# Kernel optimization log

Measured on AMD Instinct MI355X. Metric: run time of the kernel, lower is better.

The kernel has to match this reference:

```python
import jax, jax.numpy as jnp
import numpy as np

B, LQ, LK, D, H = 16, 1024, 1024, 512, 8
DK = D // H  # 64
EPS = 1e-5


def _ln(x, g, b):
    m = jnp.mean(x, axis=-1, keepdims=True)
    v = jnp.mean((x - m) ** 2, axis=-1, keepdims=True)
    return (x - m) * jax.lax.rsqrt(v + EPS) * g + b


def _rotate_every_two(x):
    # x: (..., d) with d even; pairs (x1,x2) -> (-x2, x1) interleaved
    x1 = x[..., 0::2]
    x2 = x[..., 1::2]
    return jnp.stack((-x2, x1), axis=-1).reshape(x.shape)


def setup_inputs() -> dict:
    key = jax.random.key(0)
    ks = jax.random.split(key, 16)
    s = 1.0 / np.sqrt(D)
    inp = {
        "satellite": jax.random.normal(ks[0], (B, LK, D), jnp.float32),
        "satellite_pos_embedding": jax.random.normal(ks[1], (2, B, LK, D), jnp.float32),
        "timeseries": jax.random.normal(ks[2], (B, LQ, D), jnp.float32),
        "timeseries_pos_embedding": jax.random.normal(ks[3], (2, B, LQ, D), jnp.float32),
        "ln_sat_g": jnp.ones((D,), jnp.float32),
        "ln_sat_b": jnp.zeros((D,), jnp.float32),
        "ln_ts_g": jnp.ones((D,), jnp.float32),
        "ln_ts_b": jnp.zeros((D,), jnp.float32),
        "Wv": jax.random.normal(ks[4], (D, DK), jnp.float32) * s,
        "bv": jnp.zeros((DK,), jnp.float32),
        "Wq": jax.random.normal(ks[5], (H, D, DK), jnp.float32) * s,
        "bq": jnp.zeros((H, DK), jnp.float32),
        "Wk": jax.random.normal(ks[6], (H, D, DK), jnp.float32) * s,
        "bk": jnp.zeros((H, DK), jnp.float32),
        "Wsat": jax.random.normal(ks[7], (H, D, DK), jnp.float32) * s,
        "bsat": jnp.zeros((H, DK), jnp.float32),
        "Wts": jax.random.normal(ks[8], (H, D, DK), jnp.float32) * s,
        "bts": jnp.zeros((H, DK), jnp.float32),
        "Wh": jax.random.normal(ks[9], (DK, D), jnp.float32) * (1.0 / np.sqrt(DK)),
    }
    return inp


def reference(satellite, satellite_pos_embedding, timeseries, timeseries_pos_embedding,
              ln_sat_g, ln_sat_b, ln_ts_g, ln_ts_b,
              Wv, bv, Wq, bq, Wk, bk, Wsat, bsat, Wts, bts, Wh):
    sat = _ln(satellite, ln_sat_g, ln_sat_b)      # (B,LK,D)
    ts = _ln(timeseries, ln_ts_g, ln_ts_b)        # (B,LQ,D)

    v = ts @ jnp.zeros_like(Wv) if False else sat @ Wv + bv  # (B,LK,DK), shared across heads

    # batched per-head projections
    q = jnp.einsum('bld,hdk->bhlk', ts, Wq) + bq[:, None, :]    # (B,H,LQ,DK)
    k = jnp.einsum('bld,hdk->bhlk', sat, Wk) + bk[:, None, :]   # (B,H,LK,DK)

    sin_sat = jnp.einsum('bld,hdk->bhlk', satellite_pos_embedding[0], Wsat) + bsat[:, None, :]
    cos_sat = jnp.einsum('bld,hdk->bhlk', satellite_pos_embedding[1], Wsat) + bsat[:, None, :]
    sin_ts = jnp.einsum('bld,hdk->bhlk', timeseries_pos_embedding[0], Wts) + bts[:, None, :]
    cos_ts = jnp.einsum('bld,hdk->bhlk', timeseries_pos_embedding[1], Wts) + bts[:, None, :]

    # rotary (dim_rotary == DK, so no pass-through part)
    q = q * cos_ts + _rotate_every_two(q) * sin_ts
    k = k * cos_sat + _rotate_every_two(k) * sin_sat

    scale = jnp.sqrt(jnp.asarray(DK, q.dtype))
    scores = jnp.einsum('bhqd,bhkd->bhqk', q, k) / scale        # (B,H,LQ,LK)
    attn = jax.nn.softmax(scores, axis=-1)
    head = jnp.einsum('bhqk,bkd->bhqd', attn, v)                # (B,H,LQ,DK)

    out = jnp.mean(head, axis=1) @ Wh                           # (B,LQ,D)
    attn_out = jnp.transpose(attn, (0, 2, 1, 3))                # (B,LQ,H,LK) matches torch.stack(dim=2)
    return (out, attn_out)
```

## Files before the change

kernel.cpp:

```cpp
#include <hip/hip_runtime.h>

#define OUT_OFF 8388608ull

typedef __attribute__((ext_vector_type(4))) float f32x4;
typedef __attribute__((ext_vector_type(8))) __bf16 bf16x8;
typedef __attribute__((ext_vector_type(8))) unsigned short us8;

__device__ __forceinline__ unsigned short f2b(float f) {
  return __builtin_bit_cast(unsigned short, (__bf16)f);
}
__device__ __forceinline__ float b2f(unsigned short u) {
  return (float)__builtin_bit_cast(__bf16, u);
}
__device__ __forceinline__ bf16x8 ldfrag(const unsigned short* p) {
  return __builtin_bit_cast(bf16x8, *(const us8*)p);
}
__device__ __forceinline__ f32x4 mfma16(bf16x8 a, bf16x8 b, f32x4 c) {
  return __builtin_amdgcn_mfma_f32_16x16x32_bf16(a, b, c, 0, 0, 0);
}
__device__ __forceinline__ void stage8_f32(unsigned short* dst, const float* src) {
  const f32x4 x = *(const f32x4*)src;
  const f32x4 y = *(const f32x4*)(src + 4);
  us8 v;
  v[0]=f2b(x[0]); v[1]=f2b(x[1]); v[2]=f2b(x[2]); v[3]=f2b(x[3]);
  v[4]=f2b(y[0]); v[5]=f2b(y[1]); v[6]=f2b(y[2]); v[7]=f2b(y[3]);
  *(us8*)dst = v;
}
__device__ __forceinline__ void stage8_split(unsigned short* dh, unsigned short* dl, const float* src) {
  const f32x4 x = *(const f32x4*)src;
  const f32x4 y = *(const f32x4*)(src + 4);
  us8 h, l;
  #pragma unroll
  for (int i = 0; i < 4; ++i) {
    unsigned short hv = f2b(x[i]); h[i] = hv; l[i] = f2b(x[i] - b2f(hv));
  }
  #pragma unroll
  for (int i = 0; i < 4; ++i) {
    unsigned short hv = f2b(y[i]); h[4+i] = hv; l[4+i] = f2b(y[i] - b2f(hv));
  }
  *(us8*)dh = h; *(us8*)dl = l;
}
__device__ __forceinline__ void stage8_bf(unsigned short* dst, const unsigned short* src) {
  *(us8*)dst = *(const us8*)src;
}

__global__ __launch_bounds__(256) void repack_kernel(
    const float* __restrict__ Wq, const float* __restrict__ Wk,
    const float* __restrict__ Wsat, const float* __restrict__ Wts,
    const float* __restrict__ Wv, const float* __restrict__ Wh,
    unsigned short* __restrict__ Wq_h, unsigned short* __restrict__ Wq_l,
    unsigned short* __restrict__ Wk_h, unsigned short* __restrict__ Wk_l,
    unsigned short* __restrict__ Wsat_h, unsigned short* __restrict__ Wsat_l,
    unsigned short* __restrict__ Wts_h, unsigned short* __restrict__ Wts_l,
    float* __restrict__ Wv_t, float* __restrict__ Wh_t)
{
  int i = blockIdx.x * 256 + threadIdx.x;
  if (i < 1048576) {
    int seg = i >> 18, j = i & 262143;
    int n = j >> 9, d = j & 511;
    const float* W = (seg == 0) ? Wq : (seg == 1) ? Wk : (seg == 2) ? Wsat : Wts;
    unsigned short* Oh = (seg == 0) ? Wq_h : (seg == 1) ? Wk_h : (seg == 2) ? Wsat_h : Wts_h;
    unsigned short* Ol = (seg == 0) ? Wq_l : (seg == 1) ? Wk_l : (seg == 2) ? Wsat_l : Wts_l;
    float w = W[((n >> 6) * 512 + d) * 64 + (n & 63)];
    unsigned short h = f2b(w);
    Oh[j] = h; Ol[j] = f2b(w - b2f(h));
  } else if (i < 1081344) {
    int j = i - 1048576; int dk = j >> 9, d = j & 511;
    Wv_t[j] = Wv[d * 64 + dk];
  } else if (i < 1114112) {
    int j = i - 1081344; int d = j >> 6, dk = j & 63;
    Wh_t[j] = Wh[dk * 512 + d];
  }
}

__global__ __launch_bounds__(256) void ln_kernel(
    const float* __restrict__ sat, const float* __restrict__ ts,
    const float* __restrict__ gs, const float* __restrict__ bs,
    const float* __restrict__ gt, const float* __restrict__ bt,
    unsigned short* __restrict__ sat_h, unsigned short* __restrict__ sat_l,
    unsigned short* __restrict__ ts_h, unsigned short* __restrict__ ts_l)
{
  int row = blockIdx.x;
  const float* x; unsigned short *yh, *yl; const float* g; const float* bb;
  if (row < 16384) {
    x = sat + (size_t)row * 512; yh = sat_h + (size_t)row * 512; yl = sat_l + (size_t)row * 512;
    g = gs; bb = bs;
  } else {
    int r = row - 16384;
    x = ts + (size_t)r * 512; yh = ts_h + (size_t)r * 512; yl = ts_l + (size_t)r * 512;
    g = gt; bb = bt;
  }
  int t = threadIdx.x;
  float x0 = x[t], x1 = x[t + 256];
  float s = x0 + x1, s2 = x0 * x0 + x1 * x1;
  #pragma unroll
  for (int o = 1; o < 64; o <<= 1) { s += __shfl_xor(s, o); s2 += __shfl_xor(s2, o); }
  __shared__ float red[8];
  int w = t >> 6;
  if ((t & 63) == 0) { red[w] = s; red[4 + w] = s2; }
  __syncthreads();
  float S  = red[0] + red[1] + red[2] + red[3];
  float S2 = red[4] + red[5] + red[6] + red[7];
  float mean = S * (1.f / 512.f);
  float inv = rsqrtf(S2 * (1.f / 512.f) - mean * mean + 1e-5f);
  float y0 = (x0 - mean) * inv * g[t]       + bb[t];
  float y1 = (x1 - mean) * inv * g[t + 256] + bb[t + 256];
  unsigned short h0 = f2b(y0), h1 = f2b(y1);
  yh[t] = h0;       yl[t] = f2b(y0 - b2f(h0));
  yh[t + 256] = h1; yl[t + 256] = f2b(y1 - b2f(h1));
}

__global__ __launch_bounds__(256) void proj_rope_kernel(
    const unsigned short* __restrict__ Axm_h, const unsigned short* __restrict__ Axm_l,
    const float* __restrict__ Axs, const float* __restrict__ Axc,
    const unsigned short* __restrict__ Bm_h, const unsigned short* __restrict__ Bm_l,
    const unsigned short* __restrict__ Br_h, const unsigned short* __restrict__ Br_l,
    const float* __restrict__ bm_, const float* __restrict__ br_,
    unsigned short* __restrict__ out_h, unsigned short* __restrict__ out_l)
{
  __shared__ __attribute__((aligned(16))) unsigned short
      sAmH[64*40], sAmL[64*40], sAsH[64*40], sAsL[64*40], sAcH[64*40], sAcL[64*40],
      sBmH[64*40], sBmL[64*40], sBrH[64*40], sBrL[64*40];
  const int tid = threadIdx.x;
  const int lane = tid & 63, wid = tid >> 6;
  const int wy = wid >> 1, wx = wid & 1;
  const int m0 = blockIdx.x * 64, n0 = blockIdx.y * 64;
  const int srow = tid >> 2, sc8 = (tid & 3) * 8;
  const int sidx = srow * 40 + sc8;

  f32x4 accM[2][2] = {}, accS[2][2] = {}, accC[2][2] = {};

  for (int k0 = 0; k0 < 512; k0 += 32) {
    const size_t ao = (size_t)(m0 + srow) * 512 + k0 + sc8;
    stage8_bf(&sAmH[sidx], Axm_h + ao);
    stage8_bf(&sAmL[sidx], Axm_l + ao);
    stage8_split(&sAsH[sidx], &sAsL[sidx], Axs + ao);
    stage8_split(&sAcH[sidx], &sAcL[sidx], Axc + ao);
    const size_t bo = (size_t)(n0 + srow) * 512 + k0 + sc8;
    stage8_bf(&sBmH[sidx], Bm_h + bo);
    stage8_bf(&sBmL[sidx], Bm_l + bo);
    stage8_bf(&sBrH[sidx], Br_h + bo);
    stage8_bf(&sBrL[sidx], Br_l + bo);
    __syncthreads();
    const int q8 = (lane >> 4) * 8;
    const int fm = (wy * 32 + (lane & 15)) * 40 + q8;
    const int fn = (wx * 32 + (lane & 15)) * 40 + q8;
    bf16x8 amh0 = ldfrag(&sAmH[fm]), amh1 = ldfrag(&sAmH[fm + 640]);
    bf16x8 aml0 = ldfrag(&sAmL[fm]), aml1 = ldfrag(&sAmL[fm + 640]);
    bf16x8 ash0 = ldfrag(&sAsH[fm]), ash1 = ldfrag(&sAsH[fm + 640]);
    bf16x8 asl0 = ldfrag(&sAsL[fm]), asl1 = ldfrag(&sAsL[fm + 640]);
    bf16x8 ach0 = ldfrag(&sAcH[fm]), ach1 = ldfrag(&sAcH[fm + 640]);
    bf16x8 acl0 = ldfrag(&sAcL[fm]), acl1 = ldfrag(&sAcL[fm + 640]);
    bf16x8 bmh0 = ldfrag(&sBmH[fn]), bmh1 = ldfrag(&sBmH[fn + 640]);
    bf16x8 bml0 = ldfrag(&sBmL[fn]), bml1 = ldfrag(&sBmL[fn + 640]);
    bf16x8 brh0 = ldfrag(&sBrH[fn]), brh1 = ldfrag(&sBrH[fn + 640]);
    bf16x8 brl0 = ldfrag(&sBrL[fn]), brl1 = ldfrag(&sBrL[fn + 640]);
    accM[0][0] = mfma16(amh0, bmh0, accM[0][0]); accM[0][1] = mfma16(amh0, bmh1, accM[0][1]);
    accM[1][0] = mfma16(amh1, bmh0, accM[1][0]); accM[1][1] = mfma16(amh1, bmh1, accM[1][1]);
    accM[0][0] = mfma16(amh0, bml0, accM[0][0]); accM[0][1] = mfma16(amh0, bml1, accM[0][1]);
    accM[1][0] = mfma16(amh1, bml0, accM[1][0]); accM[1][1] = mfma16(amh1, bml1, accM[1][1]);
    accM[0][0] = mfma16(aml0, bmh0, accM[0][0]); accM[0][1] = mfma16(aml0, bmh1, accM[0][1]);
    accM[1][0] = mfma16(aml1, bmh0, accM[1][0]); accM[1][1] = mfma16(aml1, bmh1, accM[1][1]);
    accS[0][0] = mfma16(ash0, brh0, accS[0][0]); accS[0][1] = mfma16(ash0, brh1, accS[0][1]);
    accS[1][0] = mfma16(ash1, brh0, accS[1][0]); accS[1][1] = mfma16(ash1, brh1, accS[1][1]);
    accS[0][0] = mfma16(ash0, brl0, accS[0][0]); accS[0][1] = mfma16(ash0, brl1, accS[0][1]);
    accS[1][0] = mfma16(ash1, brl0, accS[1][0]); accS[1][1] = mfma16(ash1, brl1, accS[1][1]);
    accS[0][0] = mfma16(asl0, brh0, accS[0][0]); accS[0][1] = mfma16(asl0, brh1, accS[0][1]);
    accS[1][0] = mfma16(asl1, brh0, accS[1][0]); accS[1][1] = mfma16(asl1, brh1, accS[1][1]);
    accC[0][0] = mfma16(ach0, brh0, accC[0][0]); accC[0][1] = mfma16(ach0, brh1, accC[0][1]);
    accC[1][0] = mfma16(ach1, brh0, accC[1][0]); accC[1][1] = mfma16(ach1, brh1, accC[1][1]);
    accC[0][0] = mfma16(ach0, brl0, accC[0][0]); accC[0][1] = mfma16(ach0, brl1, accC[0][1]);
    accC[1][0] = mfma16(ach1, brl0, accC[1][0]); accC[1][1] = mfma16(ach1, brl1, accC[1][1]);
    accC[0][0] = mfma16(acl0, brh0, accC[0][0]); accC[0][1] = mfma16(acl0, brh1, accC[0][1]);
    accC[1][0] = mfma16(acl1, brh0, accC[1][0]); accC[1][1] = mfma16(acl1, brh1, accC[1][1]);
    __syncthreads();
  }

  const int col = lane & 15, quad = lane >> 4;
  #pragma unroll
  for (int nt = 0; nt < 2; ++nt) {
    const int n = n0 + wx * 32 + nt * 16 + col;
    const float bmv = bm_[n], brv = br_[n];
    const int h = n >> 6, dk = n & 63;
    const float sgn = (n & 1) ? 1.f : -1.f;
    #pragma unroll
    for (int mt = 0; mt < 2; ++mt) {
      #pragma unroll
      for (int r = 0; r < 4; ++r) {
        float qv = accM[mt][nt][r] + bmv;
        float sv = accS[mt][nt][r] + brv;
        float cv = accC[mt][nt][r] + brv;
        float qo = __shfl_xor(qv, 1);
        float res = qv * cv + sgn * qo * sv;
        const int m = m0 + wy * 32 + mt * 16 + quad * 4 + r;
        const int b = m >> 10, l = m & 1023;
        const size_t idx = (((size_t)(b * 8 + h) * 1024 + l) << 6) + dk;
        unsigned short hv = f2b(res);
        out_h[idx] = hv;
        out_l[idx] = f2b(res - b2f(hv));
      }
    }
  }
}

__global__ __launch_bounds__(256) void scores_kernel(
    const unsigned short* __restrict__ q_h, const unsigned short* __restrict__ q_l,
    const unsigned short* __restrict__ k_h, const unsigned short* __restrict__ k_l,
    float* __restrict__ attn)
{
  __shared__ __attribute__((aligned(16))) unsigned short
      sQH[64*40], sQL[64*40], sKH[64*40], sKL[64*40];
  const int tid = threadIdx.x;
  const int lane = tid & 63, wid = tid >> 6;
  const int wy = wid >> 1, wx = wid & 1;
  const int m0 = blockIdx.x * 64, n0 = blockIdx.y * 64;
  const int z = blockIdx.z;
  const size_t base = (size_t)z << 16;
  const int srow = tid >> 2, sc8 = (tid & 3) * 8;
  const int sidx = srow * 40 + sc8;

  f32x4 acc[2][2] = {};

  for (int k0 = 0; k0 < 64; k0 += 32) {
    const size_t ao = base + (size_t)(m0 + srow) * 64 + k0 + sc8;
    stage8_bf(&sQH[sidx], q_h + ao);
    stage8_bf(&sQL[sidx], q_l + ao);
    const size_t bo = base + (size_t)(n0 + srow) * 64 + k0 + sc8;
    stage8_bf(&sKH[sidx], k_h + bo);
    stage8_bf(&sKL[sidx], k_l + bo);
    __syncthreads();
    const int q8 = (lane >> 4) * 8;
    const int fm = (wy * 32 + (lane & 15)) * 40 + q8;
    const int fn = (wx * 32 + (lane & 15)) * 40 + q8;
    bf16x8 qh0 = ldfrag(&sQH[fm]), qh1 = ldfrag(&sQH[fm + 640]);
    bf16x8 ql0 = ldfrag(&sQL[fm]), ql1 = ldfrag(&sQL[fm + 640]);
    bf16x8 kh0 = ldfrag(&sKH[fn]), kh1 = ldfrag(&sKH[fn + 640]);
    bf16x8 kl0 = ldfrag(&sKL[fn]), kl1 = ldfrag(&sKL[fn + 640]);
    acc[0][0] = mfma16(qh0, kh0, acc[0][0]); acc[0][1] = mfma16(qh0, kh1, acc[0][1]);
    acc[1][0] = mfma16(qh1, kh0, acc[1][0]); acc[1][1] = mfma16(qh1, kh1, acc[1][1]);
    acc[0][0] = mfma16(qh0, kl0, acc[0][0]); acc[0][1] = mfma16(qh0, kl1, acc[0][1]);
    acc[1][0] = mfma16(qh1, kl0, acc[1][0]); acc[1][1] = mfma16(qh1, kl1, acc[1][1]);
    acc[0][0] = mfma16(ql0, kh0, acc[0][0]); acc[0][1] = mfma16(ql0, kh1, acc[0][1]);
    acc[1][0] = mfma16(ql1, kh0, acc[1][0]); acc[1][1] = mfma16(ql1, kh1, acc[1][1]);
    __syncthreads();
  }

  const int col = lane & 15, quad = lane >> 4;
  const int b = z >> 3, h = z & 7;
  #pragma unroll
  for (int nt = 0; nt < 2; ++nt) {
    const int n = n0 + wx * 32 + nt * 16 + col;
    #pragma unroll
    for (int mt = 0; mt < 2; ++mt) {
      #pragma unroll
      for (int r = 0; r < 4; ++r) {
        const int m = m0 + wy * 32 + mt * 16 + quad * 4 + r;
        attn[((((size_t)b * 1024 + m) * 8 + h) << 10) + n] = acc[mt][nt][r] * 0.125f;
      }
    }
  }
}

enum { MODE_V = 0, MODE_PV = 2, MODE_OUT = 3 };

template<int MODE>
__global__ __launch_bounds__(256) void mfma_gemm(
    const void* __restrict__ Ap, const void* __restrict__ Bp,
    const float* __restrict__ bias, void* __restrict__ Outp)
{
  constexpr bool A_BF  = (MODE == MODE_V);
  constexpr bool B_BF  = (MODE == MODE_PV);
  constexpr int  LDA   = (MODE == MODE_V) ? 512 : (MODE == MODE_PV) ? 8192 : 64;
  constexpr int  LDB   = (MODE == MODE_V) ? 512 : (MODE == MODE_PV) ? 1024 : 64;
  constexpr int  KTOT  = (MODE == MODE_V) ? 512 : (MODE == MODE_PV) ? 1024 : 64;
  constexpr float SCALE = (MODE == MODE_V) ? 0.125f : 1.0f;

  __shared__ __attribute__((aligned(16))) unsigned short sA[64*40], sB[64*40];
  const int tid = threadIdx.x;
  const int lane = tid & 63, wid = tid >> 6;
  const int wy = wid >> 1, wx = wid & 1;
  const int m0 = blockIdx.x * 64, n0 = blockIdx.y * 64;
  const int z = blockIdx.z;
  const int srow = tid >> 2, sc8 = (tid & 3) * 8;
  const int sidx = srow * 40 + sc8;

  const float* Af = (const float*)Ap;  const unsigned short* Ab = (const unsigned short*)Ap;
  const float* Bf = (const float*)Bp;  const unsigned short* Bb = (const unsigned short*)Bp;
  size_t abase = 0, bbase = 0;
  if constexpr (MODE == MODE_PV) {
    const int b = z >> 3, kc = z & 7;
    abase = (size_t)b * (1024ull * 8192) + (size_t)kc * 1024;
    bbase = (size_t)b << 16;
  }

  f32x4 acc[2][2] = {};

  for (int k0 = 0; k0 < KTOT; k0 += 32) {
    { const size_t ao = abase + (size_t)(m0 + srow) * LDA + k0 + sc8;
      if constexpr (A_BF) stage8_bf(&sA[sidx], Ab + ao); else stage8_f32(&sA[sidx], Af + ao); }
    { const size_t bo = bbase + (size_t)(n0 + srow) * LDB + k0 + sc8;
      if constexpr (B_BF) stage8_bf(&sB[sidx], Bb + bo); else stage8_f32(&sB[sidx], Bf + bo); }
    __syncthreads();
    const int q8 = (lane >> 4) * 8;
    const int fm = (wy * 32 + (lane & 15)) * 40 + q8;
    const int fn = (wx * 32 + (lane & 15)) * 40 + q8;
    bf16x8 a0 = ldfrag(&sA[fm]), a1 = ldfrag(&sA[fm + 640]);
    bf16x8 b0 = ldfrag(&sB[fn]), b1 = ldfrag(&sB[fn + 640]);
    acc[0][0] = mfma16(a0, b0, acc[0][0]); acc[0][1] = mfma16(a0, b1, acc[0][1]);
    acc[1][0] = mfma16(a1, b0, acc[1][0]); acc[1][1] = mfma16(a1, b1, acc[1][1]);
    __syncthreads();
  }

  const int col = lane & 15, quad = lane >> 4;
  #pragma unroll
  for (int nt = 0; nt < 2; ++nt) {
    const int n = n0 + wx * 32 + nt * 16 + col;
    const float bv = bias ? bias[n] : 0.f;
    #pragma unroll
    for (int mt = 0; mt < 2; ++mt) {
      #pragma unroll
      for (int r = 0; r < 4; ++r) {
        const int m = m0 + wy * 32 + mt * 16 + quad * 4 + r;
        const float v = (acc[mt][nt][r] + bv) * SCALE;
        if constexpr (MODE == MODE_V) {
          ((unsigned short*)Outp)[((size_t)(m >> 10) << 16) + ((size_t)n << 10) + (m & 1023)] = f2b(v);
        } else if constexpr (MODE == MODE_PV) {
          const int b = z >> 3;
          atomicAdd(&((float*)Outp)[((size_t)b << 16) + m * 64 + n], v);
        } else {
          ((float*)Outp)[(size_t)m * 512 + n] = v;
        }
      }
    }
  }
}

__global__ __launch_bounds__(256) void softmax_kernel(float* __restrict__ attn)
{
  const int lane = threadIdx.x & 63, wid = threadIdx.x >> 6;
  const size_t row = (size_t)blockIdx.x * 4 + wid;
  float* p = attn + (row << 10);
  f32x4 v[4];
  #pragma unroll
  for (int i = 0; i < 4; ++i) v[i] = *(const f32x4*)(p + i * 256 + lane * 4);
  float mx = -1e30f;
  #pragma unroll
  for (int i = 0; i < 4; ++i)
    #pragma unroll
    for (int j = 0; j < 4; ++j) mx = fmaxf(mx, v[i][j]);
  #pragma unroll
  for (int o = 1; o < 64; o <<= 1) mx = fmaxf(mx, __shfl_xor(mx, o));
  float sum = 0.f;
  #pragma unroll
  for (int i = 0; i < 4; ++i)
    #pragma unroll
    for (int j = 0; j < 4; ++j) { v[i][j] = __expf(v[i][j] - mx); sum += v[i][j]; }
  #pragma unroll
  for (int o = 1; o < 64; o <<= 1) sum += __shfl_xor(sum, o);
  const float r = 1.f / sum;
  #pragma unroll
  for (int i = 0; i < 4; ++i) {
    v[i][0] *= r; v[i][1] *= r; v[i][2] *= r; v[i][3] *= r;
    *(f32x4*)(p + i * 256 + lane * 4) = v[i];
  }
}

extern "C" void kernel_launch(void* const* d_in, const int* in_sizes, int n_in,
                              void* d_out, int out_size, void* d_ws, size_t ws_size,
                              hipStream_t stream)
{
  const float* satellite  = (const float*)d_in[0];
  const float* sat_pos    = (const float*)d_in[1];
  const float* timeseries = (const float*)d_in[2];
  const float* ts_pos     = (const float*)d_in[3];
  const float* ln_sat_g   = (const float*)d_in[4];
  const float* ln_sat_b   = (const float*)d_in[5];
  const float* ln_ts_g    = (const float*)d_in[6];
  const float* ln_ts_b    = (const float*)d_in[7];
  const float* Wv  = (const float*)d_in[8];
  const float* bv  = (const float*)d_in[9];
  const float* Wq  = (const float*)d_in[10];
  const float* bq  = (const float*)d_in[11];
  const float* Wk  = (const float*)d_in[12];
  const float* bk  = (const float*)d_in[13];
  const float* Wsat= (const float*)d_in[14];
  const float* bsat= (const float*)d_in[15];
  const float* Wts = (const float*)d_in[16];
  const float* bts = (const float*)d_in[17];
  const float* Wh  = (const float*)d_in[18];

  char* ws = (char*)d_ws;
  unsigned short* sat_h = (unsigned short*)(ws + 0);
  unsigned short* sat_l = (unsigned short*)(ws + 16777216);
  unsigned short* ts_h  = (unsigned short*)(ws + 33554432);
  unsigned short* ts_l  = (unsigned short*)(ws + 50331648);
  unsigned short* q_hi  = (unsigned short*)(ws + 67108864);
  unsigned short* k_hi  = (unsigned short*)(ws + 83886080);
  unsigned short* vt    = (unsigned short*)(ws + 100663296);
  float* out_pre        = (float*)(ws + 102760448);
  char* wb = ws + 106954752;
  unsigned short* Wq_h   = (unsigned short*)(wb + 0);
  unsigned short* Wq_l   = (unsigned short*)(wb + 524288);
  unsigned short* Wk_h   = (unsigned short*)(wb + 1048576);
  unsigned short* Wk_l   = (unsigned short*)(wb + 1572864);
  unsigned short* Wsat_h = (unsigned short*)(wb + 2097152);
  unsigned short* Wsat_l = (unsigned short*)(wb + 2621440);
  unsigned short* Wts_h  = (unsigned short*)(wb + 3145728);
  unsigned short* Wts_l  = (unsigned short*)(wb + 3670016);
  float* Wv_t            = (float*)(wb + 4194304);
  float* Wh_t            = (float*)(wb + 4325376);

  float* outF = (float*)d_out;
  float* attn = outF + OUT_OFF;
  unsigned short* q_lo = (unsigned short*)d_out;
  unsigned short* k_lo = (unsigned short*)d_out + 8388608;

  repack_kernel<<<4352, 256, 0, stream>>>(Wq, Wk, Wsat, Wts, Wv, Wh,
      Wq_h, Wq_l, Wk_h, Wk_l, Wsat_h, Wsat_l, Wts_h, Wts_l, Wv_t, Wh_t);
  ln_kernel<<<32768, 256, 0, stream>>>(satellite, timeseries, ln_sat_g, ln_sat_b,
                                       ln_ts_g, ln_ts_b, sat_h, sat_l, ts_h, ts_l);
  proj_rope_kernel<<<dim3(256, 8), 256, 0, stream>>>(
      ts_h, ts_l, ts_pos, ts_pos + 8388608, Wq_h, Wq_l, Wts_h, Wts_l, bq, bts, q_hi, q_lo);
  proj_rope_kernel<<<dim3(256, 8), 256, 0, stream>>>(
      sat_h, sat_l, sat_pos, sat_pos + 8388608, Wk_h, Wk_l, Wsat_h, Wsat_l, bk, bsat, k_hi, k_lo);
  mfma_gemm<MODE_V><<<dim3(256, 1, 1), 256, 0, stream>>>(sat_h, Wv_t, bv, vt);
  scores_kernel<<<dim3(16, 16, 128), 256, 0, stream>>>(q_hi, q_lo, k_hi, k_lo, attn);
  softmax_kernel<<<32768, 256, 0, stream>>>(attn);
  hipMemsetAsync(out_pre, 0, 16384 * 64 * 4, stream);
  mfma_gemm<MODE_PV><<<dim3(16, 1, 128), 256, 0, stream>>>(attn, vt, nullptr, out_pre);
  mfma_gemm<MODE_OUT><<<dim3(256, 8, 1), 256, 0, stream>>>(out_pre, Wh_t, nullptr, outF);
}
```

Baseline: 1.497 ms.

## Fuse scores, softmax and PV into one attention kernel

Replaces the separate scores, softmax and PV GEMM kernels with one kernel per (16-query block, batch-head). It computes full score rows in registers with split-bf16 MFMAs over swizzled LDS K tiles, does the softmax with cross-wave reductions, writes the normalized attn once, and stages P as bf16 in LDS for the PV MFMA with atomic accumulation. This removes the extra read-modify-write passes over the 512MB attn tensor that the old softmax and PV steps made. In exchange it uses large LDS (48KB) and many registers per block, which may lower occupancy, and it reloads K from global memory for every 16-query block.

```diff
diff --git a/kernel.cpp b/kernel.cpp
--- a/kernel.cpp
+++ b/kernel.cpp
@@ -14,6 +14,9 @@
 }
 __device__ __forceinline__ bf16x8 ldfrag(const unsigned short* p) {
   return __builtin_bit_cast(bf16x8, *(const us8*)p);
+}
+__device__ __forceinline__ bf16x8 ldsfrag(const unsigned short* base, int byte_off) {
+  return __builtin_bit_cast(bf16x8, *(const us8*)((const char*)base + byte_off));
 }
 __device__ __forceinline__ f32x4 mfma16(bf16x8 a, bf16x8 b, f32x4 c) {
   return __builtin_amdgcn_mfma_f32_16x16x32_bf16(a, b, c, 0, 0, 0);
@@ -203,65 +206,147 @@
   }
 }
 
-__global__ __launch_bounds__(256) void scores_kernel(
+__global__ __launch_bounds__(256) void fused_attn_kernel(
     const unsigned short* __restrict__ q_h, const unsigned short* __restrict__ q_l,
     const unsigned short* __restrict__ k_h, const unsigned short* __restrict__ k_l,
-    float* __restrict__ attn)
-{
-  __shared__ __attribute__((aligned(16))) unsigned short
-      sQH[64*40], sQL[64*40], sKH[64*40], sKL[64*40];
-  const int tid = threadIdx.x;
+    const unsigned short* __restrict__ vt,
+    float* __restrict__ attn, float* __restrict__ out_pre)
+{
+  __shared__ __attribute__((aligned(16))) unsigned short sK[8192];
+  __shared__ __attribute__((aligned(16))) unsigned short sP[16384];
+  __shared__ float redM[16][4];
+  __shared__ float redS[16][4];
+
+  const int tid  = threadIdx.x;
   const int lane = tid & 63, wid = tid >> 6;
-  const int wy = wid >> 1, wx = wid & 1;
-  const int m0 = blockIdx.x * 64, n0 = blockIdx.y * 64;
-  const int z = blockIdx.z;
-  const size_t base = (size_t)z << 16;
-  const int srow = tid >> 2, sc8 = (tid & 3) * 8;
-  const int sidx = srow * 40 + sc8;
-
-  f32x4 acc[2][2] = {};
-
-  for (int k0 = 0; k0 < 64; k0 += 32) {
-    const size_t ao = base + (size_t)(m0 + srow) * 64 + k0 + sc8;
-    stage8_bf(&sQH[sidx], q_h + ao);
-    stage8_bf(&sQL[sidx], q_l + ao);
-    const size_t bo = base + (size_t)(n0 + srow) * 64 + k0 + sc8;
-    stage8_bf(&sKH[sidx], k_h + bo);
-    stage8_bf(&sKL[sidx], k_l + bo);
-    __syncthreads();
-    const int q8 = (lane >> 4) * 8;
-    const int fm = (wy * 32 + (lane & 15)) * 40 + q8;
-    const int fn = (wx * 32 + (lane & 15)) * 40 + q8;
-    bf16x8 qh0 = ldfrag(&sQH[fm]), qh1 = ldfrag(&sQH[fm + 640]);
-    bf16x8 ql0 = ldfrag(&sQL[fm]), ql1 = ldfrag(&sQL[fm + 640]);
-    bf16x8 kh0 = ldfrag(&sKH[fn]), kh1 = ldfrag(&sKH[fn + 640]);
-    bf16x8 kl0 = ldfrag(&sKL[fn]), kl1 = ldfrag(&sKL[fn + 640]);
-    acc[0][0] = mfma16(qh0, kh0, acc[0][0]); acc[0][1] = mfma16(qh0, kh1, acc[0][1]);
-    acc[1][0] = mfma16(qh1, kh0, acc[1][0]); acc[1][1] = mfma16(qh1, kh1, acc[1][1]);
-    acc[0][0] = mfma16(qh0, kl0, acc[0][0]); acc[0][1] = mfma16(qh0, kl1, acc[0][1]);
-    acc[1][0] = mfma16(qh1, kl0, acc[1][0]); acc[1][1] = mfma16(qh1, kl1, acc[1][1]);
-    acc[0][0] = mfma16(ql0, kh0, acc[0][0]); acc[0][1] = mfma16(ql0, kh1, acc[0][1]);
-    acc[1][0] = mfma16(ql1, kh0, acc[1][0]); acc[1][1] = mfma16(ql1, kh1, acc[1][1]);
-    __syncthreads();
-  }
-
-  const int col = lane & 15, quad = lane >> 4;
-  const int b = z >> 3, h = z & 7;
-  #pragma unroll
-  for (int nt = 0; nt < 2; ++nt) {
-    const int n = n0 + wx * 32 + nt * 16 + col;
-    #pragma unroll
-    for (int mt = 0; mt < 2; ++mt) {
+  const int col  = lane & 15, quad = lane >> 4;
+  const int q0   = blockIdx.x * 16;
+  const int z    = blockIdx.y;
+  const int b    = z >> 3;
+  const size_t zoff = (size_t)z << 16;
+
+  const size_t qoff = zoff + (size_t)(q0 + col) * 64 + quad * 8;
+  const bf16x8 aQh0 = ldfrag(q_h + qoff), aQh1 = ldfrag(q_h + qoff + 32);
+  const bf16x8 aQl0 = ldfrag(q_l + qoff), aQl1 = ldfrag(q_l + qoff + 32);
+
+  us8 kreg[4];
+  const unsigned short* ksrc[4];
+  int kdst[4];
+  #pragma unroll
+  for (int i = 0; i < 4; ++i) {
+    const int s = tid + i * 256;
+    const int plane = s >> 9, r = (s >> 3) & 63, c = s & 7;
+    ksrc[i] = (plane ? k_l : k_h) + zoff + (size_t)r * 64 + c * 8;
+    kdst[i] = plane * 8192 + r * 128 + ((c ^ (r & 7)) << 4);
+  }
+  #pragma unroll
+  for (int i = 0; i < 4; ++i) kreg[i] = *(const us8*)(ksrc[i]);
+
+  const int nl  = wid * 16 + col;
+  const int sx  = nl & 7;
+  const int bh0_off = nl * 128 + ((quad ^ sx) << 4);
+  const int bh1_off = nl * 128 + (((4 + quad) ^ sx) << 4);
+  const int bl0_off = 8192 + bh0_off;
+  const int bl1_off = 8192 + bh1_off;
+
+  f32x4 acc[16];
+  #pragma unroll
+  for (int kt = 0; kt < 16; ++kt) acc[kt] = (f32x4){0.f, 0.f, 0.f, 0.f};
+
+  #pragma unroll
+  for (int kt = 0; kt < 16; ++kt) {
+    __syncthreads();
+    #pragma unroll
+    for (int i = 0; i < 4; ++i) *(us8*)((char*)sK + kdst[i]) = kreg[i];
+    __syncthreads();
+    if (kt < 15) {
       #pragma unroll
-      for (int r = 0; r < 4; ++r) {
-        const int m = m0 + wy * 32 + mt * 16 + quad * 4 + r;
-        attn[((((size_t)b * 1024 + m) * 8 + h) << 10) + n] = acc[mt][nt][r] * 0.125f;
-      }
+      for (int i = 0; i < 4; ++i) kreg[i] = *(const us8*)(ksrc[i] + (kt + 1) * 4096);
     }
-  }
-}
-
-enum { MODE_V = 0, MODE_PV = 2, MODE_OUT = 3 };
+    bf16x8 bh0 = ldsfrag(sK, bh0_off), bh1 = ldsfrag(sK, bh1_off);
+    bf16x8 bl0 = ldsfrag(sK, bl0_off), bl1 = ldsfrag(sK, bl1_off);
+    acc[kt] = mfma16(aQh0, bh0, acc[kt]);
+    acc[kt] = mfma16(aQh0, bl0, acc[kt]);
+    acc[kt] = mfma16(aQl0, bh0, acc[kt]);
+    acc[kt] = mfma16(aQh1, bh1, acc[kt]);
+    acc[kt] = mfma16(aQh1, bl1, acc[kt]);
+    acc[kt] = mfma16(aQl1, bh1, acc[kt]);
+  }
+
+  float pm[4];
+  #pragma unroll
+  for (int r = 0; r < 4; ++r) pm[r] = acc[0][r];
+  #pragma unroll
+  for (int kt = 1; kt < 16; ++kt)
+    #pragma unroll
+    for (int r = 0; r < 4; ++r) pm[r] = fmaxf(pm[r], acc[kt][r]);
+  #pragma unroll
+  for (int o = 1; o < 16; o <<= 1)
+    #pragma unroll
+    for (int r = 0; r < 4; ++r) pm[r] = fmaxf(pm[r], __shfl_xor(pm[r], o));
+  if (col == 0)
+    #pragma unroll
+    for (int r = 0; r < 4; ++r) redM[quad * 4 + r][wid] = pm[r];
+  __syncthreads();
+  float M_[4];
+  #pragma unroll
+  for (int r = 0; r < 4; ++r) {
+    const float* q = redM[quad * 4 + r];
+    M_[r] = fmaxf(fmaxf(q[0], q[1]), fmaxf(q[2], q[3]));
+  }
+  float ps[4] = {0.f, 0.f, 0.f, 0.f};
+  #pragma unroll
+  for (int kt = 0; kt < 16; ++kt)
+    #pragma unroll
+    for (int r = 0; r < 4; ++r) {
+      float p = __expf((acc[kt][r] - M_[r]) * 0.125f);
+      acc[kt][r] = p; ps[r] += p;
+    }
+  #pragma unroll
+  for (int o = 1; o < 16; o <<= 1)
+    #pragma unroll
+    for (int r = 0; r < 4; ++r) ps[r] += __shfl_xor(ps[r], o);
+  if (col == 0)
+    #pragma unroll
+    for (int r = 0; r < 4; ++r) redS[quad * 4 + r][wid] = ps[r];
+  __syncthreads();
+  float rinv[4];
+  #pragma unroll
+  for (int r = 0; r < 4; ++r) {
+    const float* q = redS[quad * 4 + r];
+    rinv[r] = 1.f / (q[0] + q[1] + q[2] + q[3]);
+  }
+
+  const size_t arow = ((((size_t)b << 10) + q0) * 8 + (z & 7)) << 10;
+  #pragma unroll
+  for (int kt = 0; kt < 16; ++kt) {
+    const int cg = kt * 64 + wid * 16 + col;
+    #pragma unroll
+    for (int r = 0; r < 4; ++r) {
+      const int row = quad * 4 + r;
+      const float pn = acc[kt][r] * rinv[r];
+      attn[arow + (size_t)row * 8192 + cg] = pn;
+      *(unsigned short*)((char*)sP + ((row * 2048 + cg * 2) ^ ((row & 7) << 4))) = f2b(pn);
+    }
+  }
+  __syncthreads();
+
+  f32x4 o4 = (f32x4){0.f, 0.f, 0.f, 0.f};
+  const unsigned short* vb = vt + ((size_t)b << 16) + (size_t)(wid * 16 + col) * 1024;
+  const int prow = col * 2048;
+  const int pswz = (col & 7) << 4;
+  #pragma unroll 4
+  for (int k0 = 0; k0 < 1024; k0 += 32) {
+    bf16x8 a  = ldsfrag(sP, prow + (((k0 + quad * 8) * 2) ^ pswz));
+    bf16x8 bv = ldfrag(vb + k0 + quad * 8);
+    o4 = mfma16(a, bv, o4);
+  }
+  const size_t obase = ((size_t)b << 16) + (size_t)(q0 + quad * 4) * 64 + wid * 16 + col;
+  #pragma unroll
+  for (int r = 0; r < 4; ++r) atomicAdd(&out_pre[obase + (size_t)r * 64], o4[r]);
+}
+
+enum { MODE_V = 0, MODE_OUT = 3 };
 
 template<int MODE>
 __global__ __launch_bounds__(256) void mfma_gemm(
@@ -269,10 +354,9 @@
     const float* __restrict__ bias, void* __restrict__ Outp)
 {
   constexpr bool A_BF  = (MODE == MODE_V);
-  constexpr bool B_BF  = (MODE == MODE_PV);
-  constexpr int  LDA   = (MODE == MODE_V) ? 512 : (MODE == MODE_PV) ? 8192 : 64;
-  constexpr int  LDB   = (MODE == MODE_V) ? 512 : (MODE == MODE_PV) ? 1024 : 64;
-  constexpr int  KTOT  = (MODE == MODE_V) ? 512 : (MODE == MODE_PV) ? 1024 : 64;
+  constexpr int  LDA   = (MODE == MODE_V) ? 512 : 64;
+  constexpr int  LDB   = (MODE == MODE_V) ? 512 : 64;
+  constexpr int  KTOT  = (MODE == MODE_V) ? 512 : 64;
   constexpr float SCALE = (MODE == MODE_V) ? 0.125f : 1.0f;
 
   __shared__ __attribute__((aligned(16))) unsigned short sA[64*40], sB[64*40];
@@ -280,26 +364,19 @@
   const int lane = tid & 63, wid = tid >> 6;
   const int wy = wid >> 1, wx = wid & 1;
   const int m0 = blockIdx.x * 64, n0 = blockIdx.y * 64;
-  const int z = blockIdx.z;
   const int srow = tid >> 2, sc8 = (tid & 3) * 8;
   const int sidx = srow * 40 + sc8;
 
   const float* Af = (const float*)Ap;  const unsigned short* Ab = (const unsigned short*)Ap;
-  const float* Bf = (const float*)Bp;  const unsigned short* Bb = (const unsigned short*)Bp;
-  size_t abase = 0, bbase = 0;
-  if constexpr (MODE == MODE_PV) {
-    const int b = z >> 3, kc = z & 7;
-    abase = (size_t)b * (1024ull * 8192) + (size_t)kc * 1024;
-    bbase = (size_t)b << 16;
-  }
+  const float* Bf = (const float*)Bp;
 
   f32x4 acc[2][2] = {};
 
   for (int k0 = 0; k0 < KTOT; k0 += 32) {
-    { const size_t ao = abase + (size_t)(m0 + srow) * LDA + k0 + sc8;
+    { const size_t ao = (size_t)(m0 + srow) * LDA + k0 + sc8;
       if constexpr (A_BF) stage8_bf(&sA[sidx], Ab + ao); else stage8_f32(&sA[sidx], Af + ao); }
-    { const size_t bo = bbase + (size_t)(n0 + srow) * LDB + k0 + sc8;
-      if constexpr (B_BF) stage8_bf(&sB[sidx], Bb + bo); else stage8_f32(&sB[sidx], Bf + bo); }
+    { const size_t bo = (size_t)(n0 + srow) * LDB + k0 + sc8;
+      stage8_f32(&sB[sidx], Bf + bo); }
     __syncthreads();
     const int q8 = (lane >> 4) * 8;
     const int fm = (wy * 32 + (lane & 15)) * 40 + q8;
@@ -324,44 +401,11 @@
         const float v = (acc[mt][nt][r] + bv) * SCALE;
         if constexpr (MODE == MODE_V) {
           ((unsigned short*)Outp)[((size_t)(m >> 10) << 16) + ((size_t)n << 10) + (m & 1023)] = f2b(v);
-        } else if constexpr (MODE == MODE_PV) {
-          const int b = z >> 3;
-          atomicAdd(&((float*)Outp)[((size_t)b << 16) + m * 64 + n], v);
         } else {
           ((float*)Outp)[(size_t)m * 512 + n] = v;
         }
       }
     }
-  }
-}
-
-__global__ __launch_bounds__(256) void softmax_kernel(float* __restrict__ attn)
-{
-  const int lane = threadIdx.x & 63, wid = threadIdx.x >> 6;
-  const size_t row = (size_t)blockIdx.x * 4 + wid;
-  float* p = attn + (row << 10);
-  f32x4 v[4];
-  #pragma unroll
-  for (int i = 0; i < 4; ++i) v[i] = *(const f32x4*)(p + i * 256 + lane * 4);
-  float mx = -1e30f;
-  #pragma unroll
-  for (int i = 0; i < 4; ++i)
-    #pragma unroll
-    for (int j = 0; j < 4; ++j) mx = fmaxf(mx, v[i][j]);
-  #pragma unroll
-  for (int o = 1; o < 64; o <<= 1) mx = fmaxf(mx, __shfl_xor(mx, o));
-  float sum = 0.f;
-  #pragma unroll
-  for (int i = 0; i < 4; ++i)
-    #pragma unroll
-    for (int j = 0; j < 4; ++j) { v[i][j] = __expf(v[i][j] - mx); sum += v[i][j]; }
-  #pragma unroll
-  for (int o = 1; o < 64; o <<= 1) sum += __shfl_xor(sum, o);
-  const float r = 1.f / sum;
-  #pragma unroll
-  for (int i = 0; i < 4; ++i) {
-    v[i][0] *= r; v[i][1] *= r; v[i][2] *= r; v[i][3] *= r;
-    *(f32x4*)(p + i * 256 + lane * 4) = v[i];
   }
 }
 
@@ -424,9 +468,8 @@
   proj_rope_kernel<<<dim3(256, 8), 256, 0, stream>>>(
       sat_h, sat_l, sat_pos, sat_pos + 8388608, Wk_h, Wk_l, Wsat_h, Wsat_l, bk, bsat, k_hi, k_lo);
   mfma_gemm<MODE_V><<<dim3(256, 1, 1), 256, 0, stream>>>(sat_h, Wv_t, bv, vt);
-  scores_kernel<<<dim3(16, 16, 128), 256, 0, stream>>>(q_hi, q_lo, k_hi, k_lo, attn);
-  softmax_kernel<<<32768, 256, 0, stream>>>(attn);
   hipMemsetAsync(out_pre, 0, 16384 * 64 * 4, stream);
-  mfma_gemm<MODE_PV><<<dim3(16, 1, 128), 256, 0, stream>>>(attn, vt, nullptr, out_pre);
+  fused_attn_kernel<<<dim3(64, 128), 256, 0, stream>>>(
+      q_hi, q_lo, k_hi, k_lo, vt, attn, out_pre);
   mfma_gemm<MODE_OUT><<<dim3(256, 8, 1), 256, 0, stream>>>(out_pre, Wh_t, nullptr, outF);
 }
```

Result: faster. 1.280 ms (-14.5%).
